# Optimization experiments

Hardware: AMD Instinct MI355X
Metric: run time of the kernel (lower is better)

Reference implementation:

```python
import jax, jax.numpy as jnp
import numpy as np

H = W = 56
HID = 384
B = 16

def dct_mat(N):
    # Orthonormal DCT-II matrix: X = D @ x, idct via D.T
    n = jnp.arange(N, dtype=jnp.float32)
    k = jnp.arange(N, dtype=jnp.float32)[:, None]
    D = jnp.cos(jnp.pi * (2.0 * n + 1.0) * k / (2.0 * N)) * jnp.sqrt(2.0 / N)
    D = D.at[0].multiply(1.0 / jnp.sqrt(2.0))
    return D

def setup_inputs() -> dict:
    key = jax.random.key(0)
    ks = jax.random.split(key, 16)
    s = 0.02
    return {
        "x": jax.random.normal(ks[0], (B, HID, H, W), dtype=jnp.float32),
        "freq_embed": jax.random.normal(ks[1], (H, W, HID), dtype=jnp.float32),
        "dw_w": jax.random.normal(ks[2], (HID, 1, 3, 3), dtype=jnp.float32) * s,
        "dw_b": jnp.zeros((HID,), jnp.float32),
        "lin_w": jax.random.normal(ks[3], (2 * HID, HID), dtype=jnp.float32) * s,
        "lin_b": jnp.zeros((2 * HID,), jnp.float32),
        "vel_w": jax.random.normal(ks[4], (HID, HID), dtype=jnp.float32) * s,
        "vel_b": jnp.zeros((HID,), jnp.float32),
        "tok_w": jax.random.normal(ks[5], (HID, HID), dtype=jnp.float32) * s,
        "tok_b": jnp.zeros((HID,), jnp.float32),
        "ln_g": jnp.ones((HID,), jnp.float32),
        "ln_b": jnp.zeros((HID,), jnp.float32),
        "out_w": jax.random.normal(ks[6], (HID, HID), dtype=jnp.float32) * s,
        "out_b": jnp.zeros((HID,), jnp.float32),
        "c": jnp.ones((1,), jnp.float32),
        "alpha": jnp.ones((1,), jnp.float32) * 0.1,
    }

def reference(x, freq_embed, dw_w, dw_b, lin_w, lin_b, vel_w, vel_b,
              tok_w, tok_b, ln_g, ln_b, out_w, out_b, c, alpha):
    Bn, C, Hh, Ww = x.shape
    # depthwise 3x3 conv, padding=1
    x = jax.lax.conv_general_dilated(
        x, dw_w, (1, 1), 'SAME',
        dimension_numbers=('NCHW', 'OIHW', 'NCHW'),
        feature_group_count=C) + dw_b[None, :, None, None]
    xl = jnp.transpose(x, (0, 2, 3, 1))            # [B,H,W,C]
    xz = xl @ lin_w.T + lin_b                      # [B,H,W,2C]
    xg, z = jnp.split(xz, 2, axis=-1)
    DH, DW_ = dct_mat(Hh), dct_mat(Ww)
    x_ch = jnp.transpose(xg, (0, 3, 1, 2))         # [B,C,H,W]
    x_u0 = jnp.einsum('ih,jw,bchw->bcij', DH, DW_, x_ch)
    x_vel = xg @ vel_w.T + vel_b                   # [B,H,W,C]
    x_v0 = jnp.einsum('ih,jw,bchw->bcij', DH, DW_, jnp.transpose(x_vel, (0, 3, 1, 2)))
    # decay map exp(-(n^2+m^2)) on linspace(0,pi)
    wn = jnp.linspace(0.0, jnp.pi, Hh + 1)[:Hh][:, None]
    wm = jnp.linspace(0.0, jnp.pi, Ww + 1)[:Ww][None, :]
    decay = jnp.exp(-(wn ** 2 + wm ** 2))[None, None]
    x_u0 = x_u0 * decay
    x_v0 = x_v0 * decay
    # wave modulation from freq embedding (shared across batch)
    t = jax.nn.relu(freq_embed @ tok_w.T + tok_b)  # [H,W,C]
    t = jnp.transpose(t, (2, 0, 1))[None]          # [1,C,H,W]
    eps = 1e-6
    cos_t = jnp.cos(c[0] * t)
    sin_t = jnp.sin(c[0] * t) / (c[0] + eps)
    final = cos_t * x_u0 + sin_t * (x_v0 + 0.5 * alpha[0] * x_u0)
    x_final = jnp.einsum('hi,wj,bchw->bcij', DH, DW_, final)  # IDCT2D
    y = jnp.transpose(x_final, (0, 2, 3, 1))       # [B,H,W,C]
    mu = jnp.mean(y, axis=-1, keepdims=True)
    var = jnp.mean((y - mu) ** 2, axis=-1, keepdims=True)
    yn = (y - mu) / jnp.sqrt(var + 1e-5) * ln_g + ln_b
    gated = yn * jax.nn.silu(z)                    # [B,H,W,C]
    out = gated @ out_w.T + out_b
    return jnp.transpose(out, (0, 3, 1, 2))        # [B,C,H,W]
```

## Files before the change

kernel.cpp:

```cpp
#include <hip/hip_runtime.h>
#include <math.h>

#define HH 56
#define WS_W 56
#define HWS 3136
#define CD 384
#define BB 16
#define NROW (BB*HWS)
#define SLOT ((size_t)NROW*CD)

typedef __attribute__((ext_vector_type(8))) short bf16x8;
typedef __attribute__((ext_vector_type(4))) float f32x4;

__device__ inline ushort f2bf(float v) {
  uint u = __float_as_uint(v);
  uint r = (u + 0x7fffu + ((u >> 16) & 1u)) >> 16;
  return (ushort)r;
}
__device__ inline float bf2f(ushort h) { return __uint_as_float((uint)h << 16); }

__global__ void prep_d_k(float* __restrict__ D) {
  for (int idx = threadIdx.x; idx < HH*HH; idx += blockDim.x) {
    int k = idx / HH, n = idx % HH;
    double v = cos(3.14159265358979323846 * (2.0*n + 1.0) * k / (2.0*HH)) * sqrt(2.0/HH);
    if (k == 0) v *= 0.70710678118654752440;
    D[idx] = (float)v;
  }
}

__global__ __launch_bounds__(256) void split_w_k(
    const float* __restrict__ W, ushort* __restrict__ hi,
    ushort* __restrict__ lo, int nelem) {
  int i = blockIdx.x*256 + threadIdx.x;
  if (i >= nelem) return;
  float v = W[i];
  ushort h = f2bf(v);
  hi[i] = h;
  lo[i] = f2bf(v - bf2f(h));
}

__global__ __launch_bounds__(256) void conv_k(
    const float* __restrict__ x, const float* __restrict__ dww,
    const float* __restrict__ dwb, ushort* __restrict__ xc)
{
  __shared__ float xs[3][58][33];
  __shared__ float wgt[32][9];
  __shared__ float wb[32];
  int t = threadIdx.x;
  int c0 = blockIdx.x * 32, h = blockIdx.y, b = blockIdx.z;
  for (int idx = t; idx < 1344; idx += 256) {
    int wq = idx % 14, rem = idx / 14;
    int dy = rem % 3, ch = rem / 3;
    int gh = h + dy - 1;
    float4 v = {0.f, 0.f, 0.f, 0.f};
    if (gh >= 0 && gh < HH)
      v = *(const float4*)(x + (((size_t)b*CD + c0 + ch)*HH + gh)*WS_W + wq*4);
    int wp = wq*4 + 1;
    xs[dy][wp+0][ch] = v.x;
    xs[dy][wp+1][ch] = v.y;
    xs[dy][wp+2][ch] = v.z;
    xs[dy][wp+3][ch] = v.w;
  }
  if (t < 192) {
    int e = t & 1, dy = (t >> 1) % 3, ch = t / 6;
    xs[dy][e*57][ch] = 0.f;
  }
  for (int idx = t; idx < 288; idx += 256)
    wgt[idx/9][idx%9] = dww[(size_t)(c0 + idx/9)*9 + idx%9];
  if (t < 32) wb[t] = dwb[c0 + t];
  __syncthreads();
  int ch = t & 31, wq8 = t >> 5;
  #pragma unroll
  for (int wwi = 0; wwi < 7; ++wwi) {
    int w = wwi*8 + wq8;
    float acc = wb[ch];
    #pragma unroll
    for (int dy = 0; dy < 3; ++dy)
      #pragma unroll
      for (int dx = 0; dx < 3; ++dx)
        acc = fmaf(wgt[ch][dy*3+dx], xs[dy][w+dx][ch], acc);
    size_t oi = ((size_t)b*HWS + h*WS_W + w)*CD + c0 + ch;
    ushort hh = f2bf(acc);
    xc[oi] = hh;
    xc[SLOT + oi] = f2bf(acc - bf2f(hh));
  }
}

template<int EPI>
__global__ __launch_bounds__(256) void gemm_k(
    const float* __restrict__ A, const float* __restrict__ Bw,
    const float* __restrict__ bias, float* __restrict__ out0,
    float* __restrict__ out1, const float* __restrict__ cptr)
{
  __shared__ float As[16][68];
  __shared__ float Bs[16][68];
  int t = threadIdx.x;
  int col0 = blockIdx.x * 64;
  int row0 = blockIdx.y * 64;
  int lr = t >> 2, lk = (t & 3) * 4;
  const float* Ap = A + (size_t)(row0 + lr)*CD + lk;
  const float* Bp = Bw + (size_t)(col0 + lr)*CD + lk;
  float acc[4][4] = {};
  int tx = t & 15, ty = t >> 4;
  for (int k0 = 0; k0 < CD; k0 += 16) {
    float4 av = *(const float4*)(Ap + k0);
    float4 bv = *(const float4*)(Bp + k0);
    __syncthreads();
    As[lk+0][lr] = av.x; As[lk+1][lr] = av.y; As[lk+2][lr] = av.z; As[lk+3][lr] = av.w;
    Bs[lk+0][lr] = bv.x; Bs[lk+1][lr] = bv.y; Bs[lk+2][lr] = bv.z; Bs[lk+3][lr] = bv.w;
    __syncthreads();
    #pragma unroll
    for (int k = 0; k < 16; ++k) {
      float4 a4 = *(const float4*)&As[k][ty*4];
      float4 b4 = *(const float4*)&Bs[k][tx*4];
      float aa[4] = {a4.x, a4.y, a4.z, a4.w};
      float bbv[4] = {b4.x, b4.y, b4.z, b4.w};
      #pragma unroll
      for (int i = 0; i < 4; ++i)
        #pragma unroll
        for (int j = 0; j < 4; ++j)
          acc[i][j] = fmaf(aa[i], bbv[j], acc[i][j]);
    }
  }
  float cs = 0.f;
  if constexpr (EPI == 2) cs = cptr[0];
  #pragma unroll
  for (int i = 0; i < 4; ++i) {
    int r = row0 + ty*4 + i;
    #pragma unroll
    for (int j = 0; j < 4; ++j) {
      int cg = col0 + tx*4 + j;
      float v = acc[i][j];
      if constexpr (EPI == 2) {
        v += bias[cg];
        v = fmaxf(v, 0.f);
        int pi = r / 56, pj = r % 56;
        float wn = 3.14159265358979323846f/56.f * (float)pi;
        float wm = 3.14159265358979323846f/56.f * (float)pj;
        float dec = expf(-(wn*wn + wm*wm));
        out0[(size_t)r*CD + cg] = cosf(cs*v)*dec;
        out1[(size_t)r*CD + cg] = sinf(cs*v)/(cs + 1e-6f)*dec;
      }
    }
  }
}

template<int EPI, int ALAY>
__global__ __launch_bounds__(256, 2) void mgemm_k(
    const ushort* __restrict__ Ah_g, const ushort* __restrict__ Al_g,
    const ushort* __restrict__ Wh, const ushort* __restrict__ Wl,
    const float* __restrict__ bias,
    float* __restrict__ out0, float* __restrict__ out1,
    const ushort* __restrict__ UinH, const float* __restrict__ cosD,
    const float* __restrict__ sinD, const float* __restrict__ velb,
    const float* __restrict__ alphap)
{
  __shared__ char smem[32768];
  int t = threadIdx.x;
  int nwg = gridDim.x * gridDim.y;
  int wgid = blockIdx.y * gridDim.x + blockIdx.x;
  int cpx = nwg >> 3;
  int sw = (wgid & 7) * cpx + (wgid >> 3);
  int col0 = (sw % gridDim.x) * 128;
  int row0 = (sw / gridDim.x) * 128;

  int r = t >> 1, half = t & 1;
  int n = r & 15, rt = r >> 4, q0 = half * 2;
  const ushort* Ahp; const ushort* Alp;
  if constexpr (ALAY == 0) {
    Ahp = Ah_g + (size_t)(row0 + r)*CD + half*16;
    Alp = Al_g + (size_t)(row0 + r)*CD + half*16;
  } else {
    int rg = row0 + r; int bb = rg / HWS, p = rg % HWS;
    size_t base = ((size_t)(bb*48 + half*2)*HWS + p)*8;
    Ahp = Ah_g + base;
    Alp = Al_g + base;
  }
  const ushort* Bhp = Wh + (size_t)(col0 + r)*CD + half*16;
  const ushort* Blp = Wl + (size_t)(col0 + r)*CD + half*16;
  int aoff0 = rt*1024 + (q0*16 + n)*16;
  int aoff1 = rt*1024 + ((q0+1)*16 + n)*16;
  int boff0 = 16384 + aoff0, boff1 = 16384 + aoff1;
  int wid = t >> 6, lane = t & 63;
  int wr = wid >> 1, wc = wid & 1;
  f32x4 acc[4][4];
  #pragma unroll
  for (int i = 0; i < 4; ++i)
    #pragma unroll
    for (int j = 0; j < 4; ++j)
      acc[i][j] = (f32x4){0.f, 0.f, 0.f, 0.f};

  for (int k0 = 0; k0 < CD; k0 += 32) {
    uint4 fh0, fh1, fl0, fl1;
    if constexpr (ALAY == 0) {
      fh0 = *(const uint4*)(Ahp + k0);
      fh1 = *(const uint4*)(Ahp + k0 + 8);
      fl0 = *(const uint4*)(Alp + k0);
      fl1 = *(const uint4*)(Alp + k0 + 8);
    } else {
      size_t o = (size_t)k0 * HWS;
      fh0 = *(const uint4*)(Ahp + o);
      fh1 = *(const uint4*)(Ahp + o + HWS*8);
      fl0 = *(const uint4*)(Alp + o);
      fl1 = *(const uint4*)(Alp + o + HWS*8);
    }
    uint4 bh0 = *(const uint4*)(Bhp + k0);
    uint4 bh1 = *(const uint4*)(Bhp + k0 + 8);
    uint4 bl0 = *(const uint4*)(Blp + k0);
    uint4 bl1 = *(const uint4*)(Blp + k0 + 8);
    __syncthreads();
    *(uint4*)(smem + aoff0)        = fh0;
    *(uint4*)(smem + aoff0 + 8192) = fl0;
    *(uint4*)(smem + aoff1)        = fh1;
    *(uint4*)(smem + aoff1 + 8192) = fl1;
    *(uint4*)(smem + boff0)        = bh0;
    *(uint4*)(smem + boff0 + 8192) = bl0;
    *(uint4*)(smem + boff1)        = bh1;
    *(uint4*)(smem + boff1 + 8192) = bl1;
    __syncthreads();
    bf16x8 Ah[4], Al[4], Bh[4], Bl[4];
    #pragma unroll
    for (int i = 0; i < 4; ++i) {
      int ao = (wr*4 + i)*1024 + lane*16;
      Ah[i] = *(const bf16x8*)(smem + ao);
      Al[i] = *(const bf16x8*)(smem + ao + 8192);
      int bo = 16384 + (wc*4 + i)*1024 + lane*16;
      Bh[i] = *(const bf16x8*)(smem + bo);
      Bl[i] = *(const bf16x8*)(smem + bo + 8192);
    }
    #pragma unroll
    for (int i = 0; i < 4; ++i)
      #pragma unroll
      for (int j = 0; j < 4; ++j) {
        acc[i][j] = __builtin_amdgcn_mfma_f32_16x16x32_bf16(Ah[i], Bh[j], acc[i][j], 0, 0, 0);
        acc[i][j] = __builtin_amdgcn_mfma_f32_16x16x32_bf16(Ah[i], Bl[j], acc[i][j], 0, 0, 0);
        acc[i][j] = __builtin_amdgcn_mfma_f32_16x16x32_bf16(Al[i], Bh[j], acc[i][j], 0, 0, 0);
      }
  }

  int nn = lane & 15, qq = lane >> 4;
  float ahalf = 0.f;
  if constexpr (EPI == 1) ahalf = 0.5f * alphap[0];
  #pragma unroll
  for (int i = 0; i < 4; ++i) {
    #pragma unroll
    for (int j = 0; j < 4; ++j) {
      #pragma unroll
      for (int reg = 0; reg < 4; ++reg) {
        int rg = row0 + wr*64 + i*16 + qq*4 + reg;
        int cg = col0 + wc*64 + j*16 + nn;
        float v = acc[i][j][reg];
        if constexpr (EPI == 0) {
          v += bias[cg];
          if (cg < CD) out0[(size_t)rg*CD + cg] = v;
          else         out1[(size_t)rg*CD + cg - CD] = v;
        } else if constexpr (EPI == 1) {
          int p = rg % HWS, bidx = rg / HWS;
          size_t uidx = ((size_t)(bidx*48 + (cg >> 3))*HWS + p)*8 + (cg & 7);
          float u  = bf2f(UinH[uidx]) + bf2f(UinH[SLOT + uidx]);
          float cd = cosD[(size_t)p*CD + cg];
          float sd = sinD[(size_t)p*CD + cg];
          if (p == 0) v += 56.f * velb[cg];
          out0[uidx] = cd*u + sd*(v + ahalf*u);
        } else {
          v += bias[cg];
          int bidx = rg / HWS, hw = rg % HWS;
          out0[((size_t)bidx*CD + cg)*HWS + hw] = v;
        }
      }
    }
  }
}

template<int INV>
__global__ __launch_bounds__(256, 2) void dct2d_k(
    const float* __restrict__ in, float* __restrict__ out,
    const float* __restrict__ Dm)
{
  __shared__ float Xs[4*3364];
  __shared__ float M1[3360];
  __shared__ float M2[3360];
  int t = threadIdx.x;
  int xb = blockIdx.x;
  int cg4 = (xb & 7)*12 + (xb >> 3);
  int b = blockIdx.y;
  int cb8 = cg4 >> 1, sub4 = (cg4 & 1)*4, c0 = cg4*4;

  for (int idx = t; idx < 3136; idx += 256) {
    int r_ = idx/56, q_ = idx%56;
    float dv = Dm[r_*56 + q_];
    if (INV) { M1[r_*60 + q_] = dv; M2[q_*60 + r_] = dv; }
    else     { M1[q_*60 + r_] = dv; M2[r_*60 + q_] = dv; }
  }
  if (INV) {
    const float* Fb = in + ((size_t)(b*48 + cb8)*HWS)*8 + sub4;
    for (int p = t; p < HWS; p += 256) {
      float4 v = *(const float4*)(Fb + (size_t)p*8);
      int h = p/56, w = p%56;
      Xs[0*3364 + h*60 + w] = v.x;
      Xs[1*3364 + h*60 + w] = v.y;
      Xs[2*3364 + h*60 + w] = v.z;
      Xs[3*3364 + h*60 + w] = v.w;
    }
  } else {
    const float* inb = in + (size_t)b*HWS*CD + c0;
    for (int p = t; p < HWS; p += 256) {
      float4 v = *(const float4*)(inb + (size_t)p*CD);
      int h = p/56, w = p%56;
      Xs[0*3364 + h*60 + w] = v.x;
      Xs[1*3364 + h*60 + w] = v.y;
      Xs[2*3364 + h*60 + w] = v.z;
      Xs[3*3364 + h*60 + w] = v.w;
    }
  }
  __syncthreads();

  int ch = t >> 6, l = t & 63;
  int jg = l % 14, hg = l / 14;
  float a2[14][4];
  if (l < 56) {
    float* Xc = &Xs[ch*3364];
    float acc[14][4] = {};
    for (int w0 = 0; w0 < 56; w0 += 4) {
      float4 m0 = *(const float4*)&M1[(w0+0)*60 + jg*4];
      float4 m1 = *(const float4*)&M1[(w0+1)*60 + jg*4];
      float4 m2 = *(const float4*)&M1[(w0+2)*60 + jg*4];
      float4 m3 = *(const float4*)&M1[(w0+3)*60 + jg*4];
      #pragma unroll
      for (int ri = 0; ri < 14; ++ri) {
        float4 xv = *(const float4*)&Xc[(hg*14 + ri)*60 + w0];
        acc[ri][0] = fmaf(xv.x, m0.x, acc[ri][0]);
        acc[ri][1] = fmaf(xv.x, m0.y, acc[ri][1]);
        acc[ri][2] = fmaf(xv.x, m0.z, acc[ri][2]);
        acc[ri][3] = fmaf(xv.x, m0.w, acc[ri][3]);
        acc[ri][0] = fmaf(xv.y, m1.x, acc[ri][0]);
        acc[ri][1] = fmaf(xv.y, m1.y, acc[ri][1]);
        acc[ri][2] = fmaf(xv.y, m1.z, acc[ri][2]);
        acc[ri][3] = fmaf(xv.y, m1.w, acc[ri][3]);
        acc[ri][0] = fmaf(xv.z, m2.x, acc[ri][0]);
        acc[ri][1] = fmaf(xv.z, m2.y, acc[ri][1]);
        acc[ri][2] = fmaf(xv.z, m2.z, acc[ri][2]);
        acc[ri][3] = fmaf(xv.z, m2.w, acc[ri][3]);
        acc[ri][0] = fmaf(xv.w, m3.x, acc[ri][0]);
        acc[ri][1] = fmaf(xv.w, m3.y, acc[ri][1]);
        acc[ri][2] = fmaf(xv.w, m3.z, acc[ri][2]);
        acc[ri][3] = fmaf(xv.w, m3.w, acc[ri][3]);
      }
    }
    #pragma unroll
    for (int ri = 0; ri < 14; ++ri) {
      float4 o = {acc[ri][0], acc[ri][1], acc[ri][2], acc[ri][3]};
      *(float4*)&Xc[(hg*14 + ri)*60 + jg*4] = o;
    }
    #pragma unroll
    for (int ri = 0; ri < 14; ++ri) { a2[ri][0]=0.f; a2[ri][1]=0.f; a2[ri][2]=0.f; a2[ri][3]=0.f; }
    for (int h0 = 0; h0 < 56; h0 += 4) {
      float4 t0 = *(const float4*)&Xc[(h0+0)*60 + jg*4];
      float4 t1 = *(const float4*)&Xc[(h0+1)*60 + jg*4];
      float4 t2 = *(const float4*)&Xc[(h0+2)*60 + jg*4];
      float4 t3 = *(const float4*)&Xc[(h0+3)*60 + jg*4];
      #pragma unroll
      for (int ri = 0; ri < 14; ++ri) {
        float4 dv = *(const float4*)&M2[(hg*14 + ri)*60 + h0];
        a2[ri][0] = fmaf(dv.x, t0.x, a2[ri][0]);
        a2[ri][1] = fmaf(dv.x, t0.y, a2[ri][1]);
        a2[ri][2] = fmaf(dv.x, t0.z, a2[ri][2]);
        a2[ri][3] = fmaf(dv.x, t0.w, a2[ri][3]);
        a2[ri][0] = fmaf(dv.y, t1.x, a2[ri][0]);
        a2[ri][1] = fmaf(dv.y, t1.y, a2[ri][1]);
        a2[ri][2] = fmaf(dv.y, t1.z, a2[ri][2]);
        a2[ri][3] = fmaf(dv.y, t1.w, a2[ri][3]);
        a2[ri][0] = fmaf(dv.z, t2.x, a2[ri][0]);
        a2[ri][1] = fmaf(dv.z, t2.y, a2[ri][1]);
        a2[ri][2] = fmaf(dv.z, t2.z, a2[ri][2]);
        a2[ri][3] = fmaf(dv.z, t2.w, a2[ri][3]);
        a2[ri][0] = fmaf(dv.w, t3.x, a2[ri][0]);
        a2[ri][1] = fmaf(dv.w, t3.y, a2[ri][1]);
        a2[ri][2] = fmaf(dv.w, t3.z, a2[ri][2]);
        a2[ri][3] = fmaf(dv.w, t3.w, a2[ri][3]);
      }
    }
  }
  __syncthreads();
  if (l < 56) {
    if (INV) {
      float* Yl = Xs;
      #pragma unroll
      for (int ri = 0; ri < 14; ++ri) {
        int p = (hg*14 + ri)*56 + jg*4;
        float4 o = {a2[ri][0], a2[ri][1], a2[ri][2], a2[ri][3]};
        *(float4*)&Yl[ch*3140 + p] = o;
      }
    } else {
      ushort* Ul = (ushort*)Xs;
      #pragma unroll
      for (int ri = 0; ri < 14; ++ri) {
        int p = (hg*14 + ri)*56 + jg*4;
        ushort hs[4], ls[4];
        #pragma unroll
        for (int dj = 0; dj < 4; ++dj) {
          float v = a2[ri][dj];
          hs[dj] = f2bf(v);
          ls[dj] = f2bf(v - bf2f(hs[dj]));
        }
        uint2 hv, lv;
        hv.x = hs[0] | ((uint)hs[1] << 16); hv.y = hs[2] | ((uint)hs[3] << 16);
        lv.x = ls[0] | ((uint)ls[1] << 16); lv.y = ls[2] | ((uint)ls[3] << 16);
        *(uint2*)&Ul[ch*3136 + p] = hv;
        *(uint2*)&Ul[12544 + ch*3136 + p] = lv;
      }
    }
  }
  __syncthreads();
  if (INV) {
    const float* Yl = Xs;
    float* ob = out + (size_t)b*HWS*CD + c0;
    for (int p = t; p < HWS; p += 256) {
      float4 o = {Yl[0*3140 + p], Yl[1*3140 + p], Yl[2*3140 + p], Yl[3*3140 + p]};
      *(float4*)(ob + (size_t)p*CD) = o;
    }
  } else {
    const ushort* Ul = (const ushort*)Xs;
    ushort* og = (ushort*)out;
    size_t base = ((size_t)(b*48 + cb8)*HWS)*8 + sub4;
    for (int idx = t; idx < 2*HWS; idx += 256) {
      int pl = idx >= HWS;
      int p = pl ? idx - HWS : idx;
      ushort u0 = Ul[pl*12544 + 0*3136 + p];
      ushort u1 = Ul[pl*12544 + 1*3136 + p];
      ushort u2 = Ul[pl*12544 + 2*3136 + p];
      ushort u3 = Ul[pl*12544 + 3*3136 + p];
      uint2 v; v.x = u0 | ((uint)u1 << 16); v.y = u2 | ((uint)u3 << 16);
      *(uint2*)(og + (size_t)pl*SLOT + base + (size_t)p*8) = v;
    }
  }
}

__global__ __launch_bounds__(256) void ln_gate_k(
    const float* __restrict__ Y, const float* __restrict__ Z,
    const float* __restrict__ g, const float* __restrict__ be,
    ushort* __restrict__ out)
{
  int lane = threadIdx.x & 63, wv = threadIdx.x >> 6;
  size_t r = (size_t)blockIdx.x*4 + wv;
  const float* y = Y + r*CD;
  float v[6];
  float s = 0.f;
  #pragma unroll
  for (int q = 0; q < 6; ++q) { v[q] = y[lane + 64*q]; s += v[q]; }
  #pragma unroll
  for (int off = 32; off > 0; off >>= 1) s += __shfl_xor(s, off, 64);
  float mu = s * (1.f/384.f);
  float s2 = 0.f;
  #pragma unroll
  for (int q = 0; q < 6; ++q) { float d = v[q]-mu; s2 += d*d; }
  #pragma unroll
  for (int off = 32; off > 0; off >>= 1) s2 += __shfl_xor(s2, off, 64);
  float rs = 1.f / sqrtf(s2*(1.f/384.f) + 1e-5f);
  #pragma unroll
  for (int q = 0; q < 6; ++q) {
    int c = lane + 64*q;
    float yn = (v[q]-mu)*rs*g[c] + be[c];
    float zv = Z[r*CD + c];
    float sz = zv / (1.f + expf(-zv));
    float gv = yn*sz;
    ushort hh = f2bf(gv);
    out[r*CD + c] = hh;
    out[SLOT + r*CD + c] = f2bf(gv - bf2f(hh));
  }
}

extern "C" void kernel_launch(void* const* d_in, const int* in_sizes, int n_in,
                              void* d_out, int out_size, void* d_ws, size_t ws_size,
                              hipStream_t stream) {
  const float* x     = (const float*)d_in[0];
  const float* fe    = (const float*)d_in[1];
  const float* dw_w  = (const float*)d_in[2];
  const float* dw_b  = (const float*)d_in[3];
  const float* lin_w = (const float*)d_in[4];
  const float* lin_b = (const float*)d_in[5];
  const float* vel_w = (const float*)d_in[6];
  const float* vel_b = (const float*)d_in[7];
  const float* tok_w = (const float*)d_in[8];
  const float* tok_b = (const float*)d_in[9];
  const float* ln_g  = (const float*)d_in[10];
  const float* ln_b  = (const float*)d_in[11];
  const float* out_w = (const float*)d_in[12];
  const float* out_b = (const float*)d_in[13];
  const float* cp    = (const float*)d_in[14];
  const float* ap    = (const float*)d_in[15];

  float* ws    = (float*)d_ws;
  float* slotA = ws;
  float* slotB = ws + SLOT;
  float* slotC = ws + 2*SLOT;
  float* Dm    = ws + 3*SLOT;
  float* cosD  = Dm + 3136;
  float* sinD  = cosD + (size_t)HWS*CD;
  ushort* whi  = (ushort*)(sinD + (size_t)HWS*CD);
  ushort* wlo  = whi + 589824;

  ushort* xcH = (ushort*)slotA;
  ushort* UH  = (ushort*)slotA;
  ushort* GH  = (ushort*)slotB;

  prep_d_k<<<1, 256, 0, stream>>>(Dm);
  split_w_k<<<1152, 256, 0, stream>>>(lin_w, whi,          wlo,          294912);
  split_w_k<<< 576, 256, 0, stream>>>(vel_w, whi + 294912, wlo + 294912, 147456);
  split_w_k<<< 576, 256, 0, stream>>>(out_w, whi + 442368, wlo + 442368, 147456);

  conv_k<<<dim3(12, 56, 16), 256, 0, stream>>>(x, dw_w, dw_b, xcH);
  gemm_k<2><<<dim3(6, 49), 256, 0, stream>>>(fe, tok_w, tok_b, cosD, sinD, cp);
  mgemm_k<0,0><<<dim3(6, 392), 256, 0, stream>>>(xcH, xcH + SLOT, whi, wlo, lin_b,
      slotB, slotC, nullptr, nullptr, nullptr, nullptr, nullptr);
  dct2d_k<0><<<dim3(96, 16), 256, 0, stream>>>(slotB, slotA, Dm);
  mgemm_k<1,1><<<dim3(3, 392), 256, 0, stream>>>(UH, UH + SLOT, whi + 294912, wlo + 294912,
      nullptr, slotB, nullptr, UH, cosD, sinD, vel_b, ap);
  dct2d_k<1><<<dim3(96, 16), 256, 0, stream>>>(slotB, slotA, Dm);
  ln_gate_k<<<12544, 256, 0, stream>>>(slotA, slotC, ln_g, ln_b, GH);
  mgemm_k<3,0><<<dim3(3, 392), 256, 0, stream>>>(GH, GH + SLOT, whi + 442368, wlo + 442368,
      out_b, (float*)d_out, nullptr, nullptr, nullptr, nullptr, nullptr, nullptr);
}
```

Before: 744.3 us.

## Use 32x32x16 MFMA with swizzled LDS in GEMM; widen DCT blocks to 8 channels

The split-bf16 GEMM now computes each 64x64 warp tile with four 32x32x16 MFMA accumulators instead of sixteen 16x16x32 ones. The shared-memory staging layout is reorganised and XOR-swizzled to match the new operand fragments and to reduce bank conflicts. Separately, the DCT kernel now handles 8 channels per 512-thread block instead of 4 per 256-thread block, so each row gives full 16-byte global loads and stores. The larger DCT block uses about twice the LDS, which drops occupancy to one block per CU.

```diff
diff --git a/kernel.cpp b/kernel.cpp
--- a/kernel.cpp
+++ b/kernel.cpp
@@ -11,6 +11,7 @@
 
 typedef __attribute__((ext_vector_type(8))) short bf16x8;
 typedef __attribute__((ext_vector_type(4))) float f32x4;
+typedef __attribute__((ext_vector_type(16))) float f32x16;
 
 __device__ inline ushort f2bf(float v) {
   uint u = __float_as_uint(v);
@@ -165,7 +166,6 @@
   int row0 = (sw / gridDim.x) * 128;
 
   int r = t >> 1, half = t & 1;
-  int n = r & 15, rt = r >> 4, q0 = half * 2;
   const ushort* Ahp; const ushort* Alp;
   if constexpr (ALAY == 0) {
     Ahp = Ah_g + (size_t)(row0 + r)*CD + half*16;
@@ -178,17 +178,21 @@
   }
   const ushort* Bhp = Wh + (size_t)(col0 + r)*CD + half*16;
   const ushort* Blp = Wl + (size_t)(col0 + r)*CD + half*16;
-  int aoff0 = rt*1024 + (q0*16 + n)*16;
-  int aoff1 = rt*1024 + ((q0+1)*16 + n)*16;
-  int boff0 = 16384 + aoff0, boff1 = 16384 + aoff1;
+  int rb = r >> 5, r5 = r & 31;
+  int aoff0 = rb*2048 + half*1024 + ((r5 ^ (half << 2))*16);
+  int aoff1 = aoff0 + 512;
+  int boff0 = 16384 + aoff0, boff1 = boff0 + 512;
   int wid = t >> 6, lane = t & 63;
   int wr = wid >> 1, wc = wid & 1;
-  f32x4 acc[4][4];
-  #pragma unroll
-  for (int i = 0; i < 4; ++i)
-    #pragma unroll
-    for (int j = 0; j < 4; ++j)
-      acc[i][j] = (f32x4){0.f, 0.f, 0.f, 0.f};
+  int l5 = lane >> 5, l31 = lane & 31;
+  f32x16 acc[2][2];
+  #pragma unroll
+  for (int i = 0; i < 2; ++i)
+    #pragma unroll
+    for (int j = 0; j < 2; ++j)
+      #pragma unroll
+      for (int e = 0; e < 16; ++e)
+        acc[i][j][e] = 0.f;
 
   for (int k0 = 0; k0 < CD; k0 += 32) {
     uint4 fh0, fh1, fl0, fl1;
@@ -210,45 +214,49 @@
     uint4 bl1 = *(const uint4*)(Blp + k0 + 8);
     __syncthreads();
     *(uint4*)(smem + aoff0)        = fh0;
+    *(uint4*)(smem + aoff1)        = fh1;
     *(uint4*)(smem + aoff0 + 8192) = fl0;
-    *(uint4*)(smem + aoff1)        = fh1;
     *(uint4*)(smem + aoff1 + 8192) = fl1;
     *(uint4*)(smem + boff0)        = bh0;
+    *(uint4*)(smem + boff1)        = bh1;
     *(uint4*)(smem + boff0 + 8192) = bl0;
-    *(uint4*)(smem + boff1)        = bh1;
     *(uint4*)(smem + boff1 + 8192) = bl1;
     __syncthreads();
-    bf16x8 Ah[4], Al[4], Bh[4], Bl[4];
-    #pragma unroll
-    for (int i = 0; i < 4; ++i) {
-      int ao = (wr*4 + i)*1024 + lane*16;
-      Ah[i] = *(const bf16x8*)(smem + ao);
-      Al[i] = *(const bf16x8*)(smem + ao + 8192);
-      int bo = 16384 + (wc*4 + i)*1024 + lane*16;
-      Bh[i] = *(const bf16x8*)(smem + bo);
-      Bl[i] = *(const bf16x8*)(smem + bo + 8192);
-    }
-    #pragma unroll
-    for (int i = 0; i < 4; ++i)
-      #pragma unroll
-      for (int j = 0; j < 4; ++j) {
-        acc[i][j] = __builtin_amdgcn_mfma_f32_16x16x32_bf16(Ah[i], Bh[j], acc[i][j], 0, 0, 0);
-        acc[i][j] = __builtin_amdgcn_mfma_f32_16x16x32_bf16(Ah[i], Bl[j], acc[i][j], 0, 0, 0);
-        acc[i][j] = __builtin_amdgcn_mfma_f32_16x16x32_bf16(Al[i], Bh[j], acc[i][j], 0, 0, 0);
-      }
-  }
-
-  int nn = lane & 15, qq = lane >> 4;
+    bf16x8 Ah[2][2], Al[2][2], Bh[2][2], Bl[2][2];
+    #pragma unroll
+    for (int i = 0; i < 2; ++i)
+      #pragma unroll
+      for (int kh = 0; kh < 2; ++kh) {
+        int rsw = (l31 ^ (kh << 2))*16;
+        int ao = (wr*2 + i)*2048 + kh*1024 + l5*512 + rsw;
+        Ah[i][kh] = *(const bf16x8*)(smem + ao);
+        Al[i][kh] = *(const bf16x8*)(smem + ao + 8192);
+        int bo = 16384 + (wc*2 + i)*2048 + kh*1024 + l5*512 + rsw;
+        Bh[i][kh] = *(const bf16x8*)(smem + bo);
+        Bl[i][kh] = *(const bf16x8*)(smem + bo + 8192);
+      }
+    #pragma unroll
+    for (int i = 0; i < 2; ++i)
+      #pragma unroll
+      for (int j = 0; j < 2; ++j)
+        #pragma unroll
+        for (int kh = 0; kh < 2; ++kh) {
+          acc[i][j] = __builtin_amdgcn_mfma_f32_32x32x16_bf16(Ah[i][kh], Bh[j][kh], acc[i][j], 0, 0, 0);
+          acc[i][j] = __builtin_amdgcn_mfma_f32_32x32x16_bf16(Ah[i][kh], Bl[j][kh], acc[i][j], 0, 0, 0);
+          acc[i][j] = __builtin_amdgcn_mfma_f32_32x32x16_bf16(Al[i][kh], Bh[j][kh], acc[i][j], 0, 0, 0);
+        }
+  }
+
   float ahalf = 0.f;
   if constexpr (EPI == 1) ahalf = 0.5f * alphap[0];
   #pragma unroll
-  for (int i = 0; i < 4; ++i) {
-    #pragma unroll
-    for (int j = 0; j < 4; ++j) {
-      #pragma unroll
-      for (int reg = 0; reg < 4; ++reg) {
-        int rg = row0 + wr*64 + i*16 + qq*4 + reg;
-        int cg = col0 + wc*64 + j*16 + nn;
+  for (int i = 0; i < 2; ++i) {
+    #pragma unroll
+    for (int j = 0; j < 2; ++j) {
+      #pragma unroll
+      for (int reg = 0; reg < 16; ++reg) {
+        int rg = row0 + wr*64 + i*32 + (reg & 3) + 8*(reg >> 2) + 4*l5;
+        int cg = col0 + wc*64 + j*32 + l31;
         float v = acc[i][j][reg];
         if constexpr (EPI == 0) {
           v += bias[cg];
@@ -273,44 +281,48 @@
 }
 
 template<int INV>
-__global__ __launch_bounds__(256, 2) void dct2d_k(
+__global__ __launch_bounds__(512, 1) void dct2d_k(
     const float* __restrict__ in, float* __restrict__ out,
     const float* __restrict__ Dm)
 {
-  __shared__ float Xs[4*3364];
+  __shared__ float Xs[8*3364];
   __shared__ float M1[3360];
   __shared__ float M2[3360];
   int t = threadIdx.x;
   int xb = blockIdx.x;
-  int cg4 = (xb & 7)*12 + (xb >> 3);
+  int cg8 = (xb & 7)*6 + (xb >> 3);
   int b = blockIdx.y;
-  int cb8 = cg4 >> 1, sub4 = (cg4 & 1)*4, c0 = cg4*4;
-
-  for (int idx = t; idx < 3136; idx += 256) {
+  int c0 = cg8*8;
+
+  for (int idx = t; idx < 3136; idx += 512) {
     int r_ = idx/56, q_ = idx%56;
     float dv = Dm[r_*56 + q_];
     if (INV) { M1[r_*60 + q_] = dv; M2[q_*60 + r_] = dv; }
     else     { M1[q_*60 + r_] = dv; M2[r_*60 + q_] = dv; }
   }
   if (INV) {
-    const float* Fb = in + ((size_t)(b*48 + cb8)*HWS)*8 + sub4;
-    for (int p = t; p < HWS; p += 256) {
-      float4 v = *(const float4*)(Fb + (size_t)p*8);
+    const float* Fb = in + ((size_t)(b*48 + cg8)*HWS)*8;
+    for (int p = t; p < HWS; p += 512) {
+      float4 v0 = *(const float4*)(Fb + (size_t)p*8);
+      float4 v1 = *(const float4*)(Fb + (size_t)p*8 + 4);
       int h = p/56, w = p%56;
-      Xs[0*3364 + h*60 + w] = v.x;
-      Xs[1*3364 + h*60 + w] = v.y;
-      Xs[2*3364 + h*60 + w] = v.z;
-      Xs[3*3364 + h*60 + w] = v.w;
+      int o = h*60 + w;
+      Xs[0*3364 + o] = v0.x; Xs[1*3364 + o] = v0.y;
+      Xs[2*3364 + o] = v0.z; Xs[3*3364 + o] = v0.w;
+      Xs[4*3364 + o] = v1.x; Xs[5*3364 + o] = v1.y;
+      Xs[6*3364 + o] = v1.z; Xs[7*3364 + o] = v1.w;
     }
   } else {
     const float* inb = in + (size_t)b*HWS*CD + c0;
-    for (int p = t; p < HWS; p += 256) {
-      float4 v = *(const float4*)(inb + (size_t)p*CD);
+    for (int p = t; p < HWS; p += 512) {
+      float4 v0 = *(const float4*)(inb + (size_t)p*CD);
+      float4 v1 = *(const float4*)(inb + (size_t)p*CD + 4);
       int h = p/56, w = p%56;
-      Xs[0*3364 + h*60 + w] = v.x;
-      Xs[1*3364 + h*60 + w] = v.y;
-      Xs[2*3364 + h*60 + w] = v.z;
-      Xs[3*3364 + h*60 + w] = v.w;
+      int o = h*60 + w;
+      Xs[0*3364 + o] = v0.x; Xs[1*3364 + o] = v0.y;
+      Xs[2*3364 + o] = v0.z; Xs[3*3364 + o] = v0.w;
+      Xs[4*3364 + o] = v1.x; Xs[5*3364 + o] = v1.y;
+      Xs[6*3364 + o] = v1.z; Xs[7*3364 + o] = v1.w;
     }
   }
   __syncthreads();
@@ -407,7 +419,7 @@
         hv.x = hs[0] | ((uint)hs[1] << 16); hv.y = hs[2] | ((uint)hs[3] << 16);
         lv.x = ls[0] | ((uint)ls[1] << 16); lv.y = ls[2] | ((uint)ls[3] << 16);
         *(uint2*)&Ul[ch*3136 + p] = hv;
-        *(uint2*)&Ul[12544 + ch*3136 + p] = lv;
+        *(uint2*)&Ul[25088 + ch*3136 + p] = lv;
       }
     }
   }
@@ -415,23 +427,26 @@
   if (INV) {
     const float* Yl = Xs;
     float* ob = out + (size_t)b*HWS*CD + c0;
-    for (int p = t; p < HWS; p += 256) {
-      float4 o = {Yl[0*3140 + p], Yl[1*3140 + p], Yl[2*3140 + p], Yl[3*3140 + p]};
-      *(float4*)(ob + (size_t)p*CD) = o;
+    for (int p = t; p < HWS; p += 512) {
+      float4 o0 = {Yl[0*3140 + p], Yl[1*3140 + p], Yl[2*3140 + p], Yl[3*3140 + p]};
+      float4 o1 = {Yl[4*3140 + p], Yl[5*3140 + p], Yl[6*3140 + p], Yl[7*3140 + p]};
+      *(float4*)(ob + (size_t)p*CD) = o0;
+      *(float4*)(ob + (size_t)p*CD + 4) = o1;
     }
   } else {
     const ushort* Ul = (const ushort*)Xs;
     ushort* og = (ushort*)out;
-    size_t base = ((size_t)(b*48 + cb8)*HWS)*8 + sub4;
-    for (int idx = t; idx < 2*HWS; idx += 256) {
+    size_t base = ((size_t)(b*48 + cg8)*HWS)*8;
+    for (int idx = t; idx < 2*HWS; idx += 512) {
       int pl = idx >= HWS;
       int p = pl ? idx - HWS : idx;
-      ushort u0 = Ul[pl*12544 + 0*3136 + p];
-      ushort u1 = Ul[pl*12544 + 1*3136 + p];
-      ushort u2 = Ul[pl*12544 + 2*3136 + p];
-      ushort u3 = Ul[pl*12544 + 3*3136 + p];
-      uint2 v; v.x = u0 | ((uint)u1 << 16); v.y = u2 | ((uint)u3 << 16);
-      *(uint2*)(og + (size_t)pl*SLOT + base + (size_t)p*8) = v;
+      const ushort* U = Ul + pl*25088;
+      uint4 v;
+      v.x = U[0*3136 + p] | ((uint)U[1*3136 + p] << 16);
+      v.y = U[2*3136 + p] | ((uint)U[3*3136 + p] << 16);
+      v.z = U[4*3136 + p] | ((uint)U[5*3136 + p] << 16);
+      v.w = U[6*3136 + p] | ((uint)U[7*3136 + p] << 16);
+      *(uint4*)(og + (size_t)pl*SLOT + base + (size_t)p*8) = v;
     }
   }
 }
@@ -513,10 +528,10 @@
   gemm_k<2><<<dim3(6, 49), 256, 0, stream>>>(fe, tok_w, tok_b, cosD, sinD, cp);
   mgemm_k<0,0><<<dim3(6, 392), 256, 0, stream>>>(xcH, xcH + SLOT, whi, wlo, lin_b,
       slotB, slotC, nullptr, nullptr, nullptr, nullptr, nullptr);
-  dct2d_k<0><<<dim3(96, 16), 256, 0, stream>>>(slotB, slotA, Dm);
+  dct2d_k<0><<<dim3(48, 16), 512, 0, stream>>>(slotB, slotA, Dm);
   mgemm_k<1,1><<<dim3(3, 392), 256, 0, stream>>>(UH, UH + SLOT, whi + 294912, wlo + 294912,
       nullptr, slotB, nullptr, UH, cosD, sinD, vel_b, ap);
-  dct2d_k<1><<<dim3(96, 16), 256, 0, stream>>>(slotB, slotA, Dm);
+  dct2d_k<1><<<dim3(48, 16), 512, 0, stream>>>(slotB, slotA, Dm);
   ln_gate_k<<<12544, 256, 0, stream>>>(slotA, slotC, ln_g, ln_b, GH);
   mgemm_k<3,0><<<dim3(3, 392), 256, 0, stream>>>(GH, GH + SLOT, whi + 442368, wlo + 442368,
       out_b, (float*)d_out, nullptr, nullptr, nullptr, nullptr, nullptr, nullptr);
```

Measured after the change: 776.0 us. 4.3% more time.
